# Kernel optimization log

Hardware: AMD Instinct MI355X
Metric: run time of the kernel (lower is better)

Reference implementation:

```python
import jax, jax.numpy as jnp
import numpy as np

B, S, H = 8, 4096, 2048
TOP_K = 32


def setup_inputs() -> dict:
    key = jax.random.key(0)
    k1, k2, k3 = jax.random.split(key, 3)
    base = jax.random.normal(k1, (B, S, H), dtype=jnp.float32)
    batch_weights = jax.random.normal(k2, (B, 1, H), dtype=jnp.float32)
    intervention_positions = jax.random.randint(k3, (B, S), 0, S, dtype=jnp.int32)
    return {"base": base, "intervention_positions": intervention_positions,
            "batch_weights": batch_weights}


def reference(base, intervention_positions, batch_weights):
    # base: [B,S,H]; intervention_positions: [B,S]; batch_weights: [B,1,H]
    b, s, h = base.shape
    bidx = jnp.arange(b)[:, None]                                   # [B,1]
    # gather intervened hidden states: base[b, pos]  -> [B,S,H]
    gathered = jnp.take_along_axis(base, intervention_positions[..., None], axis=1)
    # psi(h) = ReLU(W h): rank-1 bmm with batch_weights -> [B,S]
    detect_latent = jax.nn.relu(
        jnp.einsum('bsh,bh->bs', gathered, batch_weights[:, 0, :]))
    topk_vals, topk_idx = jax.lax.top_k(detect_latent, TOP_K)       # [B,K]
    # zero out the top-k entries (scatter along last dim)
    non_topk_latents = detect_latent.at[bidx, topk_idx].set(0.0)
    # steering vector: mean(topk) * W  -> [B,1,H]
    steer = jnp.mean(topk_vals, axis=-1)[:, None, None] * batch_weights
    # scatter-add steering vector back at the intervened positions
    mixed_output = base.at[bidx, intervention_positions].add(
        jnp.broadcast_to(steer, (b, s, h)))
    return mixed_output, detect_latent, non_topk_latents
```

## Files before the change

kernel.cpp:

```cpp
#include <hip/hip_runtime.h>

#define TOPK 32

typedef float vfloat4 __attribute__((ext_vector_type(4)));

__global__ void dot_kernel(const float* __restrict__ base,
                           const float* __restrict__ bw,
                           float* __restrict__ d2,
                           int S, int H) {
    int wid  = (blockIdx.x * blockDim.x + threadIdx.x) >> 6;
    int lane = threadIdx.x & 63;
    int b = wid / S;

    const float4* row = (const float4*)(base + (size_t)wid * H);
    const float4* w4  = (const float4*)(bw + (size_t)b * H);
    int n4 = H >> 2;

    float acc = 0.f;
    #pragma unroll 8
    for (int i = lane; i < n4; i += 64) {
        float4 v = row[i];
        float4 w = w4[i];
        acc += v.x * w.x + v.y * w.y + v.z * w.z + v.w * w.w;
    }
    #pragma unroll
    for (int off = 32; off > 0; off >>= 1)
        acc += __shfl_down(acc, off, 64);

    if (lane == 0) d2[wid] = acc;
}

__global__ void topk_kernel(const float* __restrict__ d2,
                            const int* __restrict__ pos,
                            float* __restrict__ detect,
                            float* __restrict__ nontopk,
                            int* __restrict__ counts,
                            float* __restrict__ meanv,
                            int S) {
    extern __shared__ float smem[];
    float* dvals = smem;
    float* vals  = smem + S;
    int*   cnt   = (int*)(smem + 2 * S);

    int b = blockIdx.x;
    int t = threadIdx.x;
    int T = blockDim.x;

    for (int i = t; i < S; i += T) {
        dvals[i] = d2[(size_t)b * S + i];
        cnt[i] = 0;
    }
    __syncthreads();
    for (int i = t; i < S; i += T) {
        int p = pos[(size_t)b * S + i];
        float v = fmaxf(dvals[p], 0.f);
        vals[i] = v;
        detect[(size_t)b * S + i] = v;
        atomicAdd(&cnt[p], 1);
    }
    __syncthreads();

    if (t < 64) {
        int lane = t;
        float sum = 0.f;
        for (int it = 0; it < TOPK; ++it) {
            float lv = -INFINITY;
            int   li = 0x7fffffff;
            for (int c = lane * 4; c < S; c += 256) {
                float4 v = *(const float4*)&vals[c];
                if (v.x > lv) { lv = v.x; li = c; }
                if (v.y > lv) { lv = v.y; li = c + 1; }
                if (v.z > lv) { lv = v.z; li = c + 2; }
                if (v.w > lv) { lv = v.w; li = c + 3; }
            }
            #pragma unroll
            for (int off = 32; off > 0; off >>= 1) {
                float ov = __shfl_down(lv, off, 64);
                int   oi = __shfl_down(li, off, 64);
                if (ov > lv || (ov == lv && oi < li)) { lv = ov; li = oi; }
            }
            lv = __shfl(lv, 0, 64);
            li = __shfl(li, 0, 64);
            sum += lv;
            if (lane == 0) vals[li] = -INFINITY;
        }
        if (lane == 0) meanv[b] = sum / (float)TOPK;
    }
    __syncthreads();

    for (int i = t; i < S; i += T) {
        float v = vals[i];
        nontopk[(size_t)b * S + i] = (v == -INFINITY) ? 0.f : v;
        counts[(size_t)b * S + i] = cnt[i];
    }
}

__global__ void mix_kernel(const float* __restrict__ base,
                           const float* __restrict__ bw,
                           const int* __restrict__ counts,
                           const float* __restrict__ meanv,
                           float* __restrict__ mixed,
                           int S, int H) {
    int r0 = blockIdx.x << 2;
    int b  = r0 / S;
    const float4* w4 = (const float4*)(bw + (size_t)b * H);
    float mb = meanv[b];
    int n4 = H >> 2;

    for (int r = r0; r < r0 + 4; ++r) {
        float scale = (float)counts[r] * mb;
        const float4* b4 = (const float4*)(base + (size_t)r * H);
        vfloat4*      o4 = (vfloat4*)(mixed + (size_t)r * H);
        #pragma unroll 2
        for (int i = threadIdx.x; i < n4; i += blockDim.x) {
            float4 v = b4[i];
            float4 w = w4[i];
            vfloat4 o;
            o.x = v.x + scale * w.x;
            o.y = v.y + scale * w.y;
            o.z = v.z + scale * w.z;
            o.w = v.w + scale * w.w;
            __builtin_nontemporal_store(o, &o4[i]);
        }
    }
}

extern "C" void kernel_launch(void* const* d_in, const int* in_sizes, int n_in,
                              void* d_out, int out_size, void* d_ws, size_t ws_size,
                              hipStream_t stream) {
    const float* base = (const float*)d_in[0];
    const int*   pos  = (const int*)d_in[1];
    const float* bw   = (const float*)d_in[2];

    long n0 = in_sizes[0];
    long n1 = in_sizes[1];
    long n2 = in_sizes[2];
    int H = (int)(n0 / n1);
    int B = (int)(n2 / H);
    int S = (int)(n1 / B);

    float* out_mixed   = (float*)d_out;
    float* out_detect  = out_mixed + (size_t)B * S * H;
    float* out_nontopk = out_detect + (size_t)B * S;

    int*   counts = (int*)d_ws;
    float* d2     = (float*)((char*)d_ws + (size_t)B * S * sizeof(int));
    float* meanv  = (float*)((char*)d_ws + 2 * (size_t)B * S * sizeof(int));

    int nrows = B * S;
    dot_kernel<<<nrows / 4, 256, 0, stream>>>(base, bw, d2, S, H);
    topk_kernel<<<B, 256, 3 * (size_t)S * sizeof(float), stream>>>(
        d2, pos, out_detect, out_nontopk, counts, meanv, S);
    mix_kernel<<<nrows / 4, 256, 0, stream>>>(base, bw, counts, meanv, out_mixed, S, H);
}
```

Measured before the change: 191.7 us.

## Compute position histogram first and skip dot products for unreferenced rows

Adds a histogram kernel that counts how often each position is referenced, runs it before the dot-product kernel, and lets each wave exit early when its row is never gathered. With uniform random positions about a third of the rows go unreferenced, so their base reads in the dot pass are avoided. d2 entries for skipped rows stay stale, but they are never read because no position points to them. The cost is one extra small kernel launch, and the top-k kernel is slimmed because it no longer builds the counts.

```diff
diff --git a/kernel.cpp b/kernel.cpp
--- a/kernel.cpp
+++ b/kernel.cpp
@@ -4,12 +4,29 @@
 
 typedef float vfloat4 __attribute__((ext_vector_type(4)));
 
+__global__ void hist_kernel(const int* __restrict__ pos,
+                            int* __restrict__ counts,
+                            int S) {
+    extern __shared__ int cnt[];
+    int b = blockIdx.x;
+    int t = threadIdx.x;
+    for (int i = t; i < S; i += 256) cnt[i] = 0;
+    __syncthreads();
+    for (int i = t; i < S; i += 256)
+        atomicAdd(&cnt[pos[(size_t)b * S + i]], 1);
+    __syncthreads();
+    for (int i = t; i < S; i += 256)
+        counts[(size_t)b * S + i] = cnt[i];
+}
+
 __global__ void dot_kernel(const float* __restrict__ base,
                            const float* __restrict__ bw,
+                           const int* __restrict__ counts,
                            float* __restrict__ d2,
                            int S, int H) {
     int wid  = (blockIdx.x * blockDim.x + threadIdx.x) >> 6;
     int lane = threadIdx.x & 63;
+    if (counts[wid] == 0) return;
     int b = wid / S;
 
     const float4* row = (const float4*)(base + (size_t)wid * H);
@@ -34,29 +51,22 @@
                             const int* __restrict__ pos,
                             float* __restrict__ detect,
                             float* __restrict__ nontopk,
-                            int* __restrict__ counts,
                             float* __restrict__ meanv,
                             int S) {
     extern __shared__ float smem[];
     float* dvals = smem;
     float* vals  = smem + S;
-    int*   cnt   = (int*)(smem + 2 * S);
 
     int b = blockIdx.x;
     int t = threadIdx.x;
-    int T = blockDim.x;
 
-    for (int i = t; i < S; i += T) {
+    for (int i = t; i < S; i += 256)
         dvals[i] = d2[(size_t)b * S + i];
-        cnt[i] = 0;
-    }
     __syncthreads();
-    for (int i = t; i < S; i += T) {
-        int p = pos[(size_t)b * S + i];
-        float v = fmaxf(dvals[p], 0.f);
+    for (int i = t; i < S; i += 256) {
+        float v = fmaxf(dvals[pos[(size_t)b * S + i]], 0.f);
         vals[i] = v;
         detect[(size_t)b * S + i] = v;
-        atomicAdd(&cnt[p], 1);
     }
     __syncthreads();
 
@@ -88,10 +98,9 @@
     }
     __syncthreads();
 
-    for (int i = t; i < S; i += T) {
+    for (int i = t; i < S; i += 256) {
         float v = vals[i];
         nontopk[(size_t)b * S + i] = (v == -INFINITY) ? 0.f : v;
-        counts[(size_t)b * S + i] = cnt[i];
     }
 }
 
@@ -148,8 +157,9 @@
     float* meanv  = (float*)((char*)d_ws + 2 * (size_t)B * S * sizeof(int));
 
     int nrows = B * S;
-    dot_kernel<<<nrows / 4, 256, 0, stream>>>(base, bw, d2, S, H);
-    topk_kernel<<<B, 256, 3 * (size_t)S * sizeof(float), stream>>>(
-        d2, pos, out_detect, out_nontopk, counts, meanv, S);
+    hist_kernel<<<B, 256, (size_t)S * sizeof(int), stream>>>(pos, counts, S);
+    dot_kernel<<<nrows / 4, 256, 0, stream>>>(base, bw, counts, d2, S, H);
+    topk_kernel<<<B, 256, 2 * (size_t)S * sizeof(float), stream>>>(
+        d2, pos, out_detect, out_nontopk, meanv, S);
     mix_kernel<<<nrows / 4, 256, 0, stream>>>(base, bw, counts, meanv, out_mixed, S, H);
 }
```

Result: faster. 177.6 us (-7.3%).

## Fuse pipeline into persistent kernel and skip dot products for unreferenced rows

Applied to the files above, without the earlier changes.

Merges the three kernels into one persistent kernel with software grid barriers. Position counts are computed first, so dot products run only for rows that are actually gathered. While the top-k blocks work, the remaining blocks copy unreferenced rows straight to the output, and the final phase writes only the rows that receive the steering update. The aim is to remove launch overheads and avoid the full read pass over base in the dot phase, in exchange for spin-wait barriers that depend on all 1024 blocks being resident at once, plus a memset.

```diff
diff --git a/kernel.cpp b/kernel.cpp
--- a/kernel.cpp
+++ b/kernel.cpp
@@ -4,123 +4,145 @@
 
 typedef float vfloat4 __attribute__((ext_vector_type(4)));
 
-__global__ void dot_kernel(const float* __restrict__ base,
-                           const float* __restrict__ bw,
-                           float* __restrict__ d2,
-                           int S, int H) {
-    int wid  = (blockIdx.x * blockDim.x + threadIdx.x) >> 6;
-    int lane = threadIdx.x & 63;
-    int b = wid / S;
-
-    const float4* row = (const float4*)(base + (size_t)wid * H);
-    const float4* w4  = (const float4*)(bw + (size_t)b * H);
-    int n4 = H >> 2;
-
-    float acc = 0.f;
-    #pragma unroll 8
-    for (int i = lane; i < n4; i += 64) {
-        float4 v = row[i];
-        float4 w = w4[i];
-        acc += v.x * w.x + v.y * w.y + v.z * w.z + v.w * w.w;
+__device__ __forceinline__ void gbar(int* cnt, int* flag, int nblocks) {
+    __syncthreads();
+    if (threadIdx.x == 0) {
+        __threadfence();
+        int arrived = __hip_atomic_fetch_add(cnt, 1, __ATOMIC_ACQ_REL,
+                                             __HIP_MEMORY_SCOPE_AGENT);
+        if (arrived == nblocks - 1) {
+            __hip_atomic_store(flag, 1, __ATOMIC_RELEASE,
+                               __HIP_MEMORY_SCOPE_AGENT);
+        } else {
+            while (__hip_atomic_load(flag, __ATOMIC_ACQUIRE,
+                                     __HIP_MEMORY_SCOPE_AGENT) == 0)
+                __builtin_amdgcn_s_sleep(4);
+        }
+        __threadfence();
     }
-    #pragma unroll
-    for (int off = 32; off > 0; off >>= 1)
-        acc += __shfl_down(acc, off, 64);
-
-    if (lane == 0) d2[wid] = acc;
+    __syncthreads();
 }
 
-__global__ void topk_kernel(const float* __restrict__ d2,
-                            const int* __restrict__ pos,
-                            float* __restrict__ detect,
-                            float* __restrict__ nontopk,
-                            int* __restrict__ counts,
-                            float* __restrict__ meanv,
-                            int S) {
-    extern __shared__ float smem[];
-    float* dvals = smem;
-    float* vals  = smem + S;
-    int*   cnt   = (int*)(smem + 2 * S);
+__global__ __launch_bounds__(256, 4)
+void fused_kernel(const float* __restrict__ base,
+                  const int* __restrict__ pos,
+                  const float* __restrict__ bw,
+                  float* __restrict__ out_mixed,
+                  float* __restrict__ out_detect,
+                  float* __restrict__ out_nontopk,
+                  int* __restrict__ bar,
+                  int* __restrict__ counts,
+                  float* __restrict__ d2,
+                  float* __restrict__ meanv,
+                  int B, int S, int H, int nblocks) {
+    __shared__ float vals[4096];
 
-    int b = blockIdx.x;
-    int t = threadIdx.x;
-    int T = blockDim.x;
+    const int t = threadIdx.x;
+    const int nrows = B * S;
+    const int gtid = blockIdx.x * 256 + t;
+    const int nthr = nblocks * 256;
+    const int n4 = H >> 2;
 
-    for (int i = t; i < S; i += T) {
-        dvals[i] = d2[(size_t)b * S + i];
-        cnt[i] = 0;
+    for (int i = gtid; i < nrows; i += nthr) {
+        int b = i / S;
+        atomicAdd(&counts[b * S + pos[i]], 1);
     }
-    __syncthreads();
-    for (int i = t; i < S; i += T) {
-        int p = pos[(size_t)b * S + i];
-        float v = fmaxf(dvals[p], 0.f);
-        vals[i] = v;
-        detect[(size_t)b * S + i] = v;
-        atomicAdd(&cnt[p], 1);
-    }
-    __syncthreads();
+    gbar(&bar[0], &bar[8], nblocks);
 
-    if (t < 64) {
-        int lane = t;
-        float sum = 0.f;
-        for (int it = 0; it < TOPK; ++it) {
-            float lv = -INFINITY;
-            int   li = 0x7fffffff;
-            for (int c = lane * 4; c < S; c += 256) {
-                float4 v = *(const float4*)&vals[c];
-                if (v.x > lv) { lv = v.x; li = c; }
-                if (v.y > lv) { lv = v.y; li = c + 1; }
-                if (v.z > lv) { lv = v.z; li = c + 2; }
-                if (v.w > lv) { lv = v.w; li = c + 3; }
+    {
+        const int w = gtid >> 6, lane = t & 63, nw = nthr >> 6;
+        for (int row = w; row < nrows; row += nw) {
+            if (counts[row] == 0) continue;
+            const float4* rp = (const float4*)(base + (size_t)row * H);
+            const float4* wp = (const float4*)(bw + (size_t)(row / S) * H);
+            float acc = 0.f;
+            #pragma unroll 8
+            for (int i = lane; i < n4; i += 64) {
+                float4 v = rp[i];
+                float4 wv = wp[i];
+                acc += v.x * wv.x + v.y * wv.y + v.z * wv.z + v.w * wv.w;
             }
             #pragma unroll
-            for (int off = 32; off > 0; off >>= 1) {
-                float ov = __shfl_down(lv, off, 64);
-                int   oi = __shfl_down(li, off, 64);
-                if (ov > lv || (ov == lv && oi < li)) { lv = ov; li = oi; }
+            for (int off = 32; off > 0; off >>= 1)
+                acc += __shfl_down(acc, off, 64);
+            if (lane == 0) d2[row] = acc;
+        }
+    }
+    gbar(&bar[1], &bar[9], nblocks);
+
+    if (blockIdx.x < B) {
+        int b = blockIdx.x;
+        for (int i = t; i < S; i += 256) {
+            float v = fmaxf(d2[(size_t)b * S + pos[(size_t)b * S + i]], 0.f);
+            vals[i] = v;
+            out_detect[(size_t)b * S + i] = v;
+        }
+        __syncthreads();
+        if (t < 64) {
+            int lane = t;
+            float sum = 0.f;
+            for (int it = 0; it < TOPK; ++it) {
+                float lv = -INFINITY;
+                int   li = 0x7fffffff;
+                for (int c = lane * 4; c < S; c += 256) {
+                    float4 v = *(const float4*)&vals[c];
+                    if (v.x > lv) { lv = v.x; li = c; }
+                    if (v.y > lv) { lv = v.y; li = c + 1; }
+                    if (v.z > lv) { lv = v.z; li = c + 2; }
+                    if (v.w > lv) { lv = v.w; li = c + 3; }
+                }
+                #pragma unroll
+                for (int off = 32; off > 0; off >>= 1) {
+                    float ov = __shfl_down(lv, off, 64);
+                    int   oi = __shfl_down(li, off, 64);
+                    if (ov > lv || (ov == lv && oi < li)) { lv = ov; li = oi; }
+                }
+                lv = __shfl(lv, 0, 64);
+                li = __shfl(li, 0, 64);
+                sum += lv;
+                if (lane == 0) vals[li] = -INFINITY;
             }
-            lv = __shfl(lv, 0, 64);
-            li = __shfl(li, 0, 64);
-            sum += lv;
-            if (lane == 0) vals[li] = -INFINITY;
+            if (lane == 0) meanv[b] = sum / (float)TOPK;
         }
-        if (lane == 0) meanv[b] = sum / (float)TOPK;
+        __syncthreads();
+        for (int i = t; i < S; i += 256) {
+            float v = vals[i];
+            out_nontopk[(size_t)b * S + i] = (v == -INFINITY) ? 0.f : v;
+        }
+    } else {
+        for (int row = blockIdx.x - B; row < nrows; row += nblocks - B) {
+            if (counts[row] != 0) continue;
+            const float4* bp = (const float4*)(base + (size_t)row * H);
+            vfloat4*      op = (vfloat4*)(out_mixed + (size_t)row * H);
+            #pragma unroll 2
+            for (int i = t; i < n4; i += 256) {
+                float4 v = bp[i];
+                vfloat4 o;
+                o.x = v.x; o.y = v.y; o.z = v.z; o.w = v.w;
+                __builtin_nontemporal_store(o, &op[i]);
+            }
+        }
     }
-    __syncthreads();
+    gbar(&bar[2], &bar[10], nblocks);
 
-    for (int i = t; i < S; i += T) {
-        float v = vals[i];
-        nontopk[(size_t)b * S + i] = (v == -INFINITY) ? 0.f : v;
-        counts[(size_t)b * S + i] = cnt[i];
-    }
-}
-
-__global__ void mix_kernel(const float* __restrict__ base,
-                           const float* __restrict__ bw,
-                           const int* __restrict__ counts,
-                           const float* __restrict__ meanv,
-                           float* __restrict__ mixed,
-                           int S, int H) {
-    int r0 = blockIdx.x << 2;
-    int b  = r0 / S;
-    const float4* w4 = (const float4*)(bw + (size_t)b * H);
-    float mb = meanv[b];
-    int n4 = H >> 2;
-
-    for (int r = r0; r < r0 + 4; ++r) {
-        float scale = (float)counts[r] * mb;
-        const float4* b4 = (const float4*)(base + (size_t)r * H);
-        vfloat4*      o4 = (vfloat4*)(mixed + (size_t)r * H);
+    for (int row = blockIdx.x; row < nrows; row += nblocks) {
+        int c = counts[row];
+        if (c == 0) continue;
+        int b = row / S;
+        float scale = (float)c * meanv[b];
+        const float4* bp = (const float4*)(base + (size_t)row * H);
+        const float4* wp = (const float4*)(bw + (size_t)b * H);
+        vfloat4*      op = (vfloat4*)(out_mixed + (size_t)row * H);
         #pragma unroll 2
-        for (int i = threadIdx.x; i < n4; i += blockDim.x) {
-            float4 v = b4[i];
-            float4 w = w4[i];
+        for (int i = t; i < n4; i += 256) {
+            float4 v = bp[i];
+            float4 w = wp[i];
             vfloat4 o;
             o.x = v.x + scale * w.x;
             o.y = v.y + scale * w.y;
             o.z = v.z + scale * w.z;
             o.w = v.w + scale * w.w;
-            __builtin_nontemporal_store(o, &o4[i]);
+            __builtin_nontemporal_store(o, &op[i]);
         }
     }
 }
@@ -143,13 +165,16 @@
     float* out_detect  = out_mixed + (size_t)B * S * H;
     float* out_nontopk = out_detect + (size_t)B * S;
 
-    int*   counts = (int*)d_ws;
-    float* d2     = (float*)((char*)d_ws + (size_t)B * S * sizeof(int));
-    float* meanv  = (float*)((char*)d_ws + 2 * (size_t)B * S * sizeof(int));
+    int*   bar    = (int*)d_ws;
+    int*   counts = bar + 16;
+    float* d2     = (float*)(counts + (size_t)B * S);
+    float* meanv  = d2 + (size_t)B * S;
 
-    int nrows = B * S;
-    dot_kernel<<<nrows / 4, 256, 0, stream>>>(base, bw, d2, S, H);
-    topk_kernel<<<B, 256, 3 * (size_t)S * sizeof(float), stream>>>(
-        d2, pos, out_detect, out_nontopk, counts, meanv, S);
-    mix_kernel<<<nrows / 4, 256, 0, stream>>>(base, bw, counts, meanv, out_mixed, S, H);
+    int nblocks = 1024;
+
+    hipMemsetAsync(d_ws, 0, (16 + (size_t)B * S) * sizeof(int), stream);
+
+    fused_kernel<<<nblocks, 256, 0, stream>>>(
+        base, pos, bw, out_mixed, out_detect, out_nontopk,
+        bar, counts, d2, meanv, B, S, H, nblocks);
 }
```

After: 610.6 us. 3.19x slower.
